# Performance work log

Measured on AMD Instinct MI355X. Metric: run time of the kernel, lower is better.

The kernel has to match this reference:

```python
import jax, jax.numpy as jnp
import numpy as np

TEMPERATURE = 0.2

def setup_inputs() -> dict:
    key = jax.random.key(0)
    k1, k2 = jax.random.split(key)
    projected = jax.random.normal(k1, (2048, 2, 256), dtype=jnp.float32)
    predicted = jax.random.normal(k2, (2048, 4, 256), dtype=jnp.float32)
    return {"projected": projected, "predicted": predicted}

def _l2norm(x, eps=1e-12):
    n = jnp.linalg.norm(x, axis=-1, keepdims=True)
    return x / jnp.maximum(n, eps)

def reference(projected, predicted):
    # projected: [B, Vg, D], predicted: [B, Vt, D], Vt >= Vg.
    # Single-process: all_gather is identity, rank=0 -> labels = arange(B).
    B, Vg, D = projected.shape
    Vt = predicted.shape[1]
    Vl = Vt - Vg
    p = _l2norm(projected)
    q = _l2norm(predicted)
    # All pairwise similarity matrices at once: [Vg, Vt, B, B]
    logits = jnp.einsum('bid,cjd->ijbc', p, q) / TEMPERATURE
    lse = jax.nn.logsumexpr if False else jax.scipy.special.logsumexp(logits, axis=-1)  # [Vg, Vt, B]
    diag = jnp.diagonal(logits, axis1=-2, axis2=-1)                                    # [Vg, Vt, B]
    L = jnp.mean(lse - diag, axis=-1)  # per-pair CE loss, shape [Vg, Vt]
    # global terms: i != ii, both in [0, Vg)
    global_sum = jnp.sum(L[:, :Vg] * (1.0 - jnp.eye(Vg, dtype=L.dtype)))
    num_global_terms = Vg * (Vg - 1)
    global_loss = global_sum / num_global_terms if num_global_terms > 0 else jnp.float32(0.0)
    # local terms: faithful to source -> predicted columns 0..Vl-1 (not offset)
    num_local_terms = Vg * Vl
    local_sum = jnp.sum(L[:, :Vl]) if Vl > 0 else jnp.float32(0.0)
    local_loss = local_sum / num_local_terms if num_local_terms > 0 else jnp.float32(0.0)
    num_terms = num_global_terms + num_local_terms
    total = (global_sum + local_sum) / num_terms
    return (total, global_loss, local_loss)
```

## Files before the change

### kernel.cpp

```cpp
#include <hip/hip_runtime.h>
#include <hip/hip_bf16.h>
#include <hip/hip_fp8.h>
#include <stdint.h>

#define TB 2048
#define TD 256

typedef long long                                         fp8x8;
typedef __attribute__((ext_vector_type(8)))  int          int8v;
typedef __attribute__((ext_vector_type(16))) float        f32x16;

union frag32 { fp8x8 g[4]; int8v v; };

#define SQRT5 2.23606797749979f
#define SCALE1 0x7F

__global__ __launch_bounds__(256) void nnclr_prep(const float* __restrict__ proj,
                                                  const float* __restrict__ pred,
                                                  unsigned char* __restrict__ pq2) {
    const int grp = blockIdx.x;
    const int v   = blockIdx.y;
    const int t   = threadIdx.x;

    __shared__ float rowbuf[32][260];
    __shared__ float scales[32];

    #pragma unroll
    for (int it = 0; it < 8; ++it) {
        const int f = it * 256 + t;
        const int m = f >> 6, q = f & 63;
        const int b = grp * 32 + m;
        const float4* src = (v < 2) ? (const float4*)(proj + ((size_t)b * 2 + v) * TD)
                                    : (const float4*)(pred + ((size_t)b * 4 + (v - 2)) * TD);
        *(float4*)&rowbuf[m][q * 4] = src[q];
    }
    __syncthreads();
    {
        const int row = t >> 3, l8 = t & 7;
        float ss = 0.f;
        #pragma unroll
        for (int n = 0; n < 32; ++n) { const float y = rowbuf[row][l8 + 8 * n]; ss += y * y; }
        ss += __shfl_xor(ss, 1, 64);
        ss += __shfl_xor(ss, 2, 64);
        ss += __shfl_xor(ss, 4, 64);
        if (l8 == 0) scales[row] = SQRT5 / fmaxf(sqrtf(ss), 1e-12f);
    }
    __syncthreads();
    unsigned int* dst32 = (unsigned int*)(pq2 + (size_t)(v * 64 + grp) * 8192);
    #pragma unroll
    for (int it = 0; it < 8; ++it) {
        const int u   = it * 256 + t;
        const int m   = u >> 6;
        const int col = (u >> 1) & 31;
        const int e4  = u & 1;
        const float sc = scales[col];
        unsigned int w = 0;
        #pragma unroll
        for (int i = 0; i < 4; ++i) {
            const float y = rowbuf[col][m * 8 + 4 * e4 + i] * sc;
            const __hip_fp8_e4m3 f8(y);
            w |= ((unsigned int)f8.__x) << (8 * i);
        }
        dst32[u] = w;
    }
}

__global__ __launch_bounds__(256, 2) void nnclr_main(const unsigned char* __restrict__ pq2,
                                                     float* __restrict__ sPart,
                                                     float* __restrict__ dPart)
{
    const int rb = blockIdx.x, ch = blockIdx.y, pair = blockIdx.z;
    const int pi = pair >> 1, pj = pair & 1;
    const int tid = threadIdx.x, lane = tid & 63, wave = tid >> 6;
    const int cl = lane & 31, hk = lane >> 5;
    const int b0 = rb * 32;

    const fp8x8* P = (const fp8x8*)pq2;
    frag32 aF[4];
    #pragma unroll
    for (int kb = 0; kb < 4; ++kb) {
        #pragma unroll
        for (int q = 0; q < 4; ++q)
            aF[kb].g[q] = P[((pi * 64 + rb) * 32 + 8 * kb + 4 * hk + q) * 32 + cl];
    }

    float sAcc[16];
    #pragma unroll
    for (int r = 0; r < 16; ++r) sAcc[r] = 0.f;
    float d0 = 0.f;
    const int  rDiag    = (cl & 3) + 4 * (cl >> 3);
    const bool laneDiag = (((cl >> 2) & 1) == hk);

    const fp8x8* Bbase = P + (size_t)(2 + pj) * 64 * 32 * 32;
    const int cg0 = ch * 16 + wave * 4;

    #pragma unroll
    for (int cgl = 0; cgl < 4; ++cgl) {
        const int cg = cg0 + cgl;
        frag32 bf[4];
        #pragma unroll
        for (int kb = 0; kb < 4; ++kb)
            #pragma unroll
            for (int q = 0; q < 4; ++q)
                bf[kb].g[q] = Bbase[((size_t)cg * 32 + 8 * kb + 4 * hk + q) * 32 + cl];
        f32x16 acc;
        #pragma unroll
        for (int r = 0; r < 16; ++r) acc[r] = 0.f;
        #pragma unroll
        for (int kb = 0; kb < 4; ++kb)
            acc = __builtin_amdgcn_mfma_scale_f32_32x32x64_f8f6f4(
                      aF[kb].v, bf[kb].v, acc, 0, 0, 0, SCALE1, 0, SCALE1);
        const bool diagCG = (cg == rb);
        #pragma unroll
        for (int r = 0; r < 16; ++r) {
            const float v0 = acc[r];
            sAcc[r] += __expf(v0 - 5.0f);
            if (diagCG) {
                const bool m = laneDiag && (r == rDiag);
                d0 += m ? v0 : 0.f;
            }
        }
    }

    #pragma unroll
    for (int r = 0; r < 16; ++r) {
        float s0 = sAcc[r];
        #pragma unroll
        for (int msk = 1; msk < 32; msk <<= 1) s0 += __shfl_xor(s0, msk, 64);
        sAcc[r] = s0;
    }

    __shared__ float sArr[4][32];
    __shared__ float dArr[4][32];
    if (cl == 0) {
        #pragma unroll
        for (int r = 0; r < 16; ++r) {
            const int rowl = (r & 3) + 8 * (r >> 2) + 4 * hk;
            sArr[wave][rowl] = sAcc[r];
        }
    }
    if (laneDiag) dArr[wave][cl] = d0;
    __syncthreads();
    if (tid < 32) {
        float s = 0.f, d = 0.f;
        #pragma unroll
        for (int w = 0; w < 4; ++w) { s += sArr[w][tid]; d += dArr[w][tid]; }
        const int b = b0 + tid;
        sPart[((size_t)pair * TB + b) * 4 + ch] = s;
        dPart[((size_t)pair * TB + b) * 4 + ch] = d;
    }
}

__global__ __launch_bounds__(1024) void nnclr_final(const float* __restrict__ sPart,
                                                    const float* __restrict__ dPart,
                                                    float* __restrict__ out) {
    const int tid = threadIdx.x;
    float acc[4] = {0.f, 0.f, 0.f, 0.f};
    #pragma unroll
    for (int k = 0; k < 8; ++k) {
        const int item = k * 1024 + tid;
        const float4 sv = ((const float4*)sPart)[item];
        const float4 dv = ((const float4*)dPart)[item];
        const float s = (sv.x + sv.y) + (sv.z + sv.w);
        const float d = (dv.x + dv.y) + (dv.z + dv.w);
        acc[k >> 1] += 5.0f + logf(s) - d;
    }
    __shared__ float red[16][4];
    const int lane = tid & 63, wave = tid >> 6;
    #pragma unroll
    for (int p = 0; p < 4; ++p) {
        #pragma unroll
        for (int m = 1; m < 64; m <<= 1) acc[p] += __shfl_xor(acc[p], m, 64);
    }
    if (lane == 0) {
        #pragma unroll
        for (int p = 0; p < 4; ++p) red[wave][p] = acc[p];
    }
    __syncthreads();
    if (tid == 0) {
        float L[4];
        #pragma unroll
        for (int p = 0; p < 4; ++p) {
            float a = 0.f;
            for (int w = 0; w < 16; ++w) a += red[w][p];
            L[p] = a / (float)TB;
        }
        const float gs = L[1] + L[2];
        const float ls = L[0] + L[1] + L[2] + L[3];
        out[0] = (gs + ls) / 6.0f;
        out[1] = gs * 0.5f;
        out[2] = ls * 0.25f;
    }
}

extern "C" void kernel_launch(void* const* d_in, const int* in_sizes, int n_in,
                              void* d_out, int out_size, void* d_ws, size_t ws_size,
                              hipStream_t stream) {
    const float* projected = (const float*)d_in[0];
    const float* predicted = (const float*)d_in[1];

    unsigned char* pq2 = (unsigned char*)d_ws;
    float* sPart = (float*)((char*)d_ws + 4u * 1024u * 1024u);
    float* dPart = sPart + (size_t)4 * TB * 4;
    float* out = (float*)d_out;

    dim3 gprep(64, 4);
    nnclr_prep<<<gprep, 256, 0, stream>>>(projected, predicted, pq2);
    dim3 gmain(64, 4, 4);
    nnclr_main<<<gmain, 256, 0, stream>>>(pq2, sPart, dPart);
    nnclr_final<<<1, 1024, 0, stream>>>(sPart, dPart, out);
}
```

Measured before the change: 27.35 us.

## Share B tiles across waves via double-buffered LDS with async global-to-LDS loads

The main kernel's work split changes so each wave owns its own 32-row A block and the four waves share each B column tile. That tile is staged into LDS with global_load_lds, double-buffered so the next tile loads while MFMAs run on the current one. The column dimension is split into 8 chunks instead of 4, so the partial-sum layout and the final reduction become 8-wide. The aim is to cut redundant global B loads and hide their latency, at the cost of a block-wide barrier every iteration and more partial sums to reduce.

```diff
diff --git a/kernel.cpp b/kernel.cpp
--- a/kernel.cpp
+++ b/kernel.cpp
@@ -18,10 +18,7 @@
 __global__ __launch_bounds__(256) void nnclr_prep(const float* __restrict__ proj,
                                                   const float* __restrict__ pred,
                                                   unsigned char* __restrict__ pq2) {
-    const int grp = blockIdx.x;
-    const int v   = blockIdx.y;
-    const int t   = threadIdx.x;
-
+    const int grp = blockIdx.x, v = blockIdx.y, t = threadIdx.x;
     __shared__ float rowbuf[32][260];
     __shared__ float scales[32];
 
@@ -49,10 +46,8 @@
     unsigned int* dst32 = (unsigned int*)(pq2 + (size_t)(v * 64 + grp) * 8192);
     #pragma unroll
     for (int it = 0; it < 8; ++it) {
-        const int u   = it * 256 + t;
-        const int m   = u >> 6;
-        const int col = (u >> 1) & 31;
-        const int e4  = u & 1;
+        const int u = it * 256 + t;
+        const int m = u >> 6, col = (u >> 1) & 31, e4 = u & 1;
         const float sc = scales[col];
         unsigned int w = 0;
         #pragma unroll
@@ -69,20 +64,23 @@
                                                      float* __restrict__ sPart,
                                                      float* __restrict__ dPart)
 {
-    const int rb = blockIdx.x, ch = blockIdx.y, pair = blockIdx.z;
+    const int rbq = blockIdx.x, ch = blockIdx.y, pair = blockIdx.z;
     const int pi = pair >> 1, pj = pair & 1;
     const int tid = threadIdx.x, lane = tid & 63, wave = tid >> 6;
     const int cl = lane & 31, hk = lane >> 5;
-    const int b0 = rb * 32;
+    const int rbW = rbq * 4 + wave;
+
+    __shared__ __align__(16) unsigned char bbuf[2][8192];
+    __shared__ float sArr[4][32];
+    __shared__ float dArr[4][32];
 
     const fp8x8* P = (const fp8x8*)pq2;
     frag32 aF[4];
     #pragma unroll
-    for (int kb = 0; kb < 4; ++kb) {
+    for (int kb = 0; kb < 4; ++kb)
         #pragma unroll
         for (int q = 0; q < 4; ++q)
-            aF[kb].g[q] = P[((pi * 64 + rb) * 32 + 8 * kb + 4 * hk + q) * 32 + cl];
-    }
+            aF[kb].g[q] = P[((pi * 64 + rbW) * 32 + 8 * kb + 4 * hk + q) * 32 + cl];
 
     float sAcc[16];
     #pragma unroll
@@ -91,18 +89,34 @@
     const int  rDiag    = (cl & 3) + 4 * (cl >> 3);
     const bool laneDiag = (((cl >> 2) & 1) == hk);
 
-    const fp8x8* Bbase = P + (size_t)(2 + pj) * 64 * 32 * 32;
-    const int cg0 = ch * 16 + wave * 4;
-
-    #pragma unroll
-    for (int cgl = 0; cgl < 4; ++cgl) {
-        const int cg = cg0 + cgl;
+    const unsigned char* Bbytes = pq2 + (size_t)(2 + pj) * 524288;
+
+    #define STAGE(buf, c)                                                          \
+        {                                                                          \
+            const unsigned char* src_ = Bbytes + ((size_t)(ch * 8 + (c))) * 8192;  \
+            _Pragma("unroll")                                                      \
+            for (int l = 0; l < 2; ++l) {                                          \
+                const int off = l * 4096 + tid * 16;                               \
+                __builtin_amdgcn_global_load_lds(                                  \
+                    (const __attribute__((address_space(1))) unsigned int*)(src_ + off), \
+                    (__attribute__((address_space(3))) unsigned int*)(&bbuf[buf][0] + off), \
+                    16, 0, 0);                                                     \
+            }                                                                      \
+        }
+
+    STAGE(0, 0);
+    __syncthreads();
+
+    #pragma unroll
+    for (int c = 0; c < 8; ++c) {
+        if (c < 7) STAGE((c + 1) & 1, c + 1);
+        const fp8x8* L = (const fp8x8*)&bbuf[c & 1][0];
         frag32 bf[4];
         #pragma unroll
         for (int kb = 0; kb < 4; ++kb)
             #pragma unroll
             for (int q = 0; q < 4; ++q)
-                bf[kb].g[q] = Bbase[((size_t)cg * 32 + 8 * kb + 4 * hk + q) * 32 + cl];
+                bf[kb].g[q] = L[(8 * kb + 4 * hk + q) * 32 + cl];
         f32x16 acc;
         #pragma unroll
         for (int r = 0; r < 16; ++r) acc[r] = 0.f;
@@ -110,7 +124,8 @@
         for (int kb = 0; kb < 4; ++kb)
             acc = __builtin_amdgcn_mfma_scale_f32_32x32x64_f8f6f4(
                       aF[kb].v, bf[kb].v, acc, 0, 0, 0, SCALE1, 0, SCALE1);
-        const bool diagCG = (cg == rb);
+        const int cg = ch * 8 + c;
+        const bool diagCG = (cg == rbW);
         #pragma unroll
         for (int r = 0; r < 16; ++r) {
             const float v0 = acc[r];
@@ -120,6 +135,7 @@
                 d0 += m ? v0 : 0.f;
             }
         }
+        __syncthreads();
     }
 
     #pragma unroll
@@ -129,9 +145,6 @@
         for (int msk = 1; msk < 32; msk <<= 1) s0 += __shfl_xor(s0, msk, 64);
         sAcc[r] = s0;
     }
-
-    __shared__ float sArr[4][32];
-    __shared__ float dArr[4][32];
     if (cl == 0) {
         #pragma unroll
         for (int r = 0; r < 16; ++r) {
@@ -141,14 +154,13 @@
     }
     if (laneDiag) dArr[wave][cl] = d0;
     __syncthreads();
-    if (tid < 32) {
-        float s = 0.f, d = 0.f;
-        #pragma unroll
-        for (int w = 0; w < 4; ++w) { s += sArr[w][tid]; d += dArr[w][tid]; }
-        const int b = b0 + tid;
-        sPart[((size_t)pair * TB + b) * 4 + ch] = s;
-        dPart[((size_t)pair * TB + b) * 4 + ch] = d;
-    }
+    if (tid < 128) {
+        const int w = tid >> 5, row = tid & 31;
+        const int b = (rbq * 4 + w) * 32 + row;
+        sPart[((size_t)pair * TB + b) * 8 + ch] = sArr[w][row];
+        dPart[((size_t)pair * TB + b) * 8 + ch] = dArr[w][row];
+    }
+    #undef STAGE
 }
 
 __global__ __launch_bounds__(1024) void nnclr_final(const float* __restrict__ sPart,
@@ -159,10 +171,12 @@
     #pragma unroll
     for (int k = 0; k < 8; ++k) {
         const int item = k * 1024 + tid;
-        const float4 sv = ((const float4*)sPart)[item];
-        const float4 dv = ((const float4*)dPart)[item];
-        const float s = (sv.x + sv.y) + (sv.z + sv.w);
-        const float d = (dv.x + dv.y) + (dv.z + dv.w);
+        const float4 s0 = ((const float4*)sPart)[item * 2];
+        const float4 s1 = ((const float4*)sPart)[item * 2 + 1];
+        const float4 e0 = ((const float4*)dPart)[item * 2];
+        const float4 e1 = ((const float4*)dPart)[item * 2 + 1];
+        const float s = ((s0.x + s0.y) + (s0.z + s0.w)) + ((s1.x + s1.y) + (s1.z + s1.w));
+        const float d = ((e0.x + e0.y) + (e0.z + e0.w)) + ((e1.x + e1.y) + (e1.z + e1.w));
         acc[k >> 1] += 5.0f + logf(s) - d;
     }
     __shared__ float red[16][4];
@@ -201,12 +215,12 @@
 
     unsigned char* pq2 = (unsigned char*)d_ws;
     float* sPart = (float*)((char*)d_ws + 4u * 1024u * 1024u);
-    float* dPart = sPart + (size_t)4 * TB * 4;
+    float* dPart = sPart + (size_t)4 * TB * 8;
     float* out = (float*)d_out;
 
     dim3 gprep(64, 4);
     nnclr_prep<<<gprep, 256, 0, stream>>>(projected, predicted, pq2);
-    dim3 gmain(64, 4, 4);
+    dim3 gmain(16, 8, 4);
     nnclr_main<<<gmain, 256, 0, stream>>>(pq2, sPart, dPart);
     nnclr_final<<<1, 1024, 0, stream>>>(sPart, dPart, out);
 }
```

Measured after the change: 32.45 us. 1.19x slower.
